# Optimization experiments

Measured on AMD Instinct MI355X. Metric: run time of the kernel, lower is better.

## Reference

```python
import jax, jax.numpy as jnp
import numpy as np

H = 128  # hidden_size = dims[0]
F = 64   # input_size = input_shape[1]
L = 3    # num_layers = len(dims)
B, T = 128, 512


def _gru_layer(x, w_ih, w_hh, b_ih, b_hh):
    """PyTorch-style GRU layer. x: [S, N, in]. Returns (ys [S,N,H], h_T [N,H])."""
    # Precompute input projections for all steps at once: [S, N, 3H]
    px = jnp.einsum('sni,gi->sng', x, w_ih) + b_ih

    def step(h, p):
        gh = h @ w_hh.T + b_hh            # [N, 3H]
        pr, pz, pn = jnp.split(p, 3, axis=-1)
        gr, gz, gn = jnp.split(gh, 3, axis=-1)
        r = jax.nn.sigmoid(pr + gr)
        z = jax.nn.sigmoid(pz + gz)
        n = jnp.tanh(pn + r * gn)
        h_new = (1.0 - z) * n + z * h
        return h_new, h_new

    h0 = jnp.zeros((x.shape[1], w_hh.shape[1]), dtype=x.dtype)
    hT, ys = jax.lax.scan(step, h0, px)
    return ys, hT


def setup_inputs() -> dict:
    key = jax.random.key(0)
    ks = jax.random.split(key, 1 + 4 * L)
    d = {"inp": jax.random.normal(ks[0], (B, T, F), dtype=jnp.float32)}
    k = 1.0 / np.sqrt(H)  # torch default uniform init bound
    for l in range(L):
        in_dim = F if l == 0 else H
        d[f"w_ih_{l}"] = jax.random.uniform(ks[1 + 4 * l + 0], (3 * H, in_dim), jnp.float32, -k, k)
        d[f"w_hh_{l}"] = jax.random.uniform(ks[1 + 4 * l + 1], (3 * H, H), jnp.float32, -k, k)
        d[f"b_ih_{l}"] = jax.random.uniform(ks[1 + 4 * l + 2], (3 * H,), jnp.float32, -k, k)
        d[f"b_hh_{l}"] = jax.random.uniform(ks[1 + 4 * l + 3], (3 * H,), jnp.float32, -k, k)
    return d


def reference(inp, w_ih_0, w_hh_0, b_ih_0, b_hh_0,
              w_ih_1, w_hh_1, b_ih_1, b_hh_1,
              w_ih_2, w_hh_2, b_ih_2, b_hh_2):
    shape = inp.shape
    # torch: reshape to [-1, T, F]; nn.GRU here has batch_first=False (positional-arg bug),
    # so the scan runs over dim 0 (length B) with dim 1 (T) as the GRU batch.
    x = inp.reshape(-1, shape[-2], shape[-1])  # [S=B, N=T, F]
    layers = [(w_ih_0, w_hh_0, b_ih_0, b_hh_0),
              (w_ih_1, w_hh_1, b_ih_1, b_hh_1),
              (w_ih_2, w_hh_2, b_ih_2, b_hh_2)]
    for w_ih, w_hh, b_ih, b_hh in layers:
        x, _ = _gru_layer(x, w_ih, w_hh, b_ih, b_hh)
    # final=False branch: reshape per-step outputs to shape[:-1] + [-1]
    return x.reshape(shape[:-1] + (-1,))
```

## Files before the change

kernel.cpp:

```cpp
#include <hip/hip_runtime.h>

namespace {

constexpr int NTH = 512;
constexpr int NB  = 512;
constexpr int HID = 128;
constexpr int G3  = 384;
constexpr int SS  = 128;
constexpr int CH  = 20;

typedef float f32x2 __attribute__((ext_vector_type(2)));
typedef float f32x4 __attribute__((ext_vector_type(4)));

__device__ __forceinline__ void pk_fma_acc(f32x2& acc, f32x2 a, f32x2 b) {
    asm("v_pk_fma_f32 %0, %1, %2, %0" : "+v"(acc) : "v"(a), "v"(b));
}

template <int CTRL>
__device__ __forceinline__ float add_dpp(float v) {
    int moved = __builtin_amdgcn_update_dpp(0, __float_as_int(v), CTRL, 0xf, 0xf, true);
    return v + __int_as_float(moved);
}

__device__ __forceinline__ float wave_red8(float v) {
    v = add_dpp<0x111>(v);
    v = add_dpp<0x112>(v);
    v = add_dpp<0x114>(v);
    return v;
}

__device__ __forceinline__ float dot4acc(float4 a, float4 b, float acc) {
    acc = fmaf(a.x, b.x, acc);
    acc = fmaf(a.y, b.y, acc);
    acc = fmaf(a.z, b.z, acc);
    acc = fmaf(a.w, b.w, acc);
    return acc;
}

__device__ __forceinline__ float fsigmoid(float x) {
    x = fminf(fmaxf(x, -30.f), 30.f);
    return 1.f / (1.f + __expf(-x));
}

__device__ __forceinline__ float ftanh(float x) {
    x = fminf(fmaxf(x, -15.f), 15.f);
    const float e = __expf(2.f * x);
    return 1.f - 2.f / (e + 1.f);
}

constexpr int BKG = 32;
constexpr int TSTR = 132;

__global__ __launch_bounds__(256, 4) void px_gemm(
    const float* __restrict__ A,
    const float* __restrict__ W,
    const float* __restrict__ bih,
    const float* __restrict__ bhh,
    float* __restrict__ px,
    int kin)
{
    __shared__ __align__(16) float At[BKG * TSTR];
    __shared__ __align__(16) float Wt[BKG * TSTR];

    const int tid = threadIdx.x;
    const int m0  = blockIdx.x * 128;
    const int g0  = blockIdx.y * 128;
    const int tr  = tid >> 4;
    const int tc  = tid & 15;

    f32x2 acc2[8][4];
    #pragma unroll
    for (int i = 0; i < 8; ++i)
        #pragma unroll
        for (int j = 0; j < 4; ++j) acc2[i][j] = f32x2{0.f, 0.f};

    const int srow = tid >> 3;
    const int sf4  = (tid & 7) * 4;

    for (int kt = 0; kt < kin; kt += BKG) {
        #pragma unroll
        for (int p = 0; p < 4; ++p) {
            const int r = p * 32 + srow;
            const float4 va = *reinterpret_cast<const float4*>(A + (size_t)(m0 + r) * kin + kt + sf4);
            At[(sf4 + 0) * TSTR + r] = va.x;
            At[(sf4 + 1) * TSTR + r] = va.y;
            At[(sf4 + 2) * TSTR + r] = va.z;
            At[(sf4 + 3) * TSTR + r] = va.w;
            const float4 vw = *reinterpret_cast<const float4*>(W + (size_t)(g0 + r) * kin + kt + sf4);
            Wt[(sf4 + 0) * TSTR + r] = vw.x;
            Wt[(sf4 + 1) * TSTR + r] = vw.y;
            Wt[(sf4 + 2) * TSTR + r] = vw.z;
            Wt[(sf4 + 3) * TSTR + r] = vw.w;
        }
        __syncthreads();

        #pragma unroll 8
        for (int kk = 0; kk < BKG; ++kk) {
            const float4 a0 = *reinterpret_cast<const float4*>(&At[kk * TSTR + tr * 8]);
            const float4 a1 = *reinterpret_cast<const float4*>(&At[kk * TSTR + tr * 8 + 4]);
            const float4 w0 = *reinterpret_cast<const float4*>(&Wt[kk * TSTR + tc * 8]);
            const float4 w1 = *reinterpret_cast<const float4*>(&Wt[kk * TSTR + tc * 8 + 4]);
            const f32x2 wp[4] = { f32x2{w0.x, w0.y}, f32x2{w0.z, w0.w},
                                  f32x2{w1.x, w1.y}, f32x2{w1.z, w1.w} };
            const float ar[8] = { a0.x, a0.y, a0.z, a0.w, a1.x, a1.y, a1.z, a1.w };
            #pragma unroll
            for (int i = 0; i < 8; ++i) {
                const f32x2 av = f32x2{ar[i], ar[i]};
                #pragma unroll
                for (int j = 0; j < 4; ++j)
                    pk_fma_acc(acc2[i][j], av, wp[j]);
            }
        }
        __syncthreads();
    }

    const int gbase = g0 + tc * 8;
    const bool addz = (g0 < 256);
    float4 b0 = *reinterpret_cast<const float4*>(bih + gbase);
    float4 b1 = *reinterpret_cast<const float4*>(bih + gbase + 4);
    if (addz) {
        const float4 h0 = *reinterpret_cast<const float4*>(bhh + gbase);
        const float4 h1 = *reinterpret_cast<const float4*>(bhh + gbase + 4);
        b0.x += h0.x; b0.y += h0.y; b0.z += h0.z; b0.w += h0.w;
        b1.x += h1.x; b1.y += h1.y; b1.z += h1.z; b1.w += h1.w;
    }
    #pragma unroll
    for (int i = 0; i < 8; ++i) {
        const int m = m0 + tr * 8 + i;
        float4 o0, o1;
        o0.x = acc2[i][0].x + b0.x; o0.y = acc2[i][0].y + b0.y;
        o0.z = acc2[i][1].x + b0.z; o0.w = acc2[i][1].y + b0.w;
        o1.x = acc2[i][2].x + b1.x; o1.y = acc2[i][2].y + b1.y;
        o1.z = acc2[i][3].x + b1.z; o1.w = acc2[i][3].y + b1.w;
        *reinterpret_cast<float4*>(px + (size_t)m * G3 + gbase)     = o0;
        *reinterpret_cast<float4*>(px + (size_t)m * G3 + gbase + 4) = o1;
    }
}

__global__ __launch_bounds__(NTH, 4) void gru_rec(
    const float* __restrict__ px,
    const float* __restrict__ whh,
    const float* __restrict__ bhh,
    float* __restrict__ yd)
{
    __shared__ __align__(16) float hb[8 * CH];
    __shared__ float ghl[G3];
    __shared__ float bhn[HID];

    const int tid  = threadIdx.x;
    const int kgrp = tid & 7;
    const int gt   = tid >> 3;
    const int g0   = gt * 6;
    const int row  = blockIdx.x;

    f32x4 wv[24];
    #pragma unroll
    for (int gg = 0; gg < 6; ++gg)
        #pragma unroll
        for (int q = 0; q < 4; ++q)
            wv[gg * 4 + q] = *reinterpret_cast<const f32x4*>(
                whh + (size_t)(g0 + gg) * HID + kgrp * 16 + q * 4);
    #pragma unroll
    for (int i = 0; i < 24; ++i) asm volatile("" : "+v"(wv[i]));

    for (int i = tid; i < HID; i += NTH) bhn[i] = bhh[256 + i];
    for (int i = tid; i < 8 * CH; i += NTH) hb[i] = 0.f;
    __syncthreads();

    float pxr = 0.f, pxz = 0.f, pxn = 0.f;
    if (tid < HID) {
        const float* p0 = px + (size_t)row * G3 + tid;
        pxr = p0[0]; pxz = p0[128]; pxn = p0[256];
    }

    for (int s = 0; s < SS; ++s) {
        if (tid >= 128 && tid < 256) {
            const int j = tid - 128;
            if (s > 0)
                yd[((size_t)(s - 1) * NB + row) * HID + j] = hb[(j >> 4) * CH + (j & 15)];
        }
        float nxr = 0.f, nxz = 0.f, nxn = 0.f;
        if (tid < HID && s + 1 < SS) {
            const float* p1 = px + ((size_t)(s + 1) * NB + row) * G3 + tid;
            nxr = p1[0]; nxz = p1[128]; nxn = p1[256];
        }

        f32x2 acc[6];
        #pragma unroll
        for (int gg = 0; gg < 6; ++gg) acc[gg] = f32x2{0.f, 0.f};
        #pragma unroll
        for (int q = 0; q < 4; ++q) {
            const f32x4 h4 = *reinterpret_cast<const f32x4*>(&hb[kgrp * CH + q * 4]);
            const f32x2 hlo = h4.xy;
            const f32x2 hhi = h4.zw;
            #pragma unroll
            for (int gg = 0; gg < 6; ++gg) {
                pk_fma_acc(acc[gg], hlo, wv[gg * 4 + q].xy);
                pk_fma_acc(acc[gg], hhi, wv[gg * 4 + q].zw);
            }
        }
        #pragma unroll
        for (int gg = 0; gg < 6; ++gg) {
            const float r = wave_red8(acc[gg].x + acc[gg].y);
            if (kgrp == 7) ghl[g0 + gg] = r;
        }
        __syncthreads();

        if (tid < HID) {
            const float ghr = ghl[tid];
            const float ghz = ghl[tid + 128];
            const float ghn = ghl[tid + 256] + bhn[tid];
            const float r  = fsigmoid(pxr + ghr);
            const float z  = fsigmoid(pxz + ghz);
            const float nn = ftanh(pxn + r * ghn);
            const int hoff = (tid >> 4) * CH + (tid & 15);
            const float hold = hb[hoff];
            hb[hoff] = (1.f - z) * nn + z * hold;
            pxr = nxr; pxz = nxz; pxn = nxn;
        }
        __syncthreads();
    }

    if (tid >= 128 && tid < 256) {
        const int j = tid - 128;
        yd[((size_t)(SS - 1) * NB + row) * HID + j] = hb[(j >> 4) * CH + (j & 15)];
    }
}

__global__ __launch_bounds__(NTH) void gru3_fused(
    const float* __restrict__ xin,
    const float* __restrict__ wih0, const float* __restrict__ whh0,
    const float* __restrict__ bih0, const float* __restrict__ bhh0,
    const float* __restrict__ wih1, const float* __restrict__ whh1,
    const float* __restrict__ bih1, const float* __restrict__ bhh1,
    const float* __restrict__ wih2, const float* __restrict__ whh2,
    const float* __restrict__ bih2, const float* __restrict__ bhh2,
    float* __restrict__ out)
{
    __shared__ __align__(16) float xb[2][2 * 8 * CH];
    __shared__ __align__(16) float hb[2 * 8 * CH];
    __shared__ float pxl[2][G3];
    __shared__ float ghl[2][G3];
    __shared__ float bsum[2 * HID];
    __shared__ float bin_[HID];
    __shared__ float bhn_[HID];

    const int tid  = threadIdx.x;
    const int kgrp = tid & 7;
    const int gt   = tid >> 3;
    const int g0   = gt * 6;
    const int row0 = blockIdx.x * 2;

    float4 wih[6][4];
    float4 whh[6][4];

    for (int layer = 0; layer < 3; ++layer) {
        const float *wi, *wh, *bi, *bh, *xs;
        float* yd;
        int kin;
        if (layer == 0)      { wi = wih0; wh = whh0; bi = bih0; bh = bhh0; xs = xin; yd = out; kin = 64;  }
        else if (layer == 1) { wi = wih1; wh = whh1; bi = bih1; bh = bhh1; xs = out; yd = out; kin = HID; }
        else                 { wi = wih2; wh = whh2; bi = bih2; bh = bhh2; xs = out; yd = out; kin = HID; }

        #pragma unroll
        for (int gg = 0; gg < 6; ++gg) {
            const int g = g0 + gg;
            #pragma unroll
            for (int q = 0; q < 4; ++q) {
                const int k = kgrp * 16 + q * 4;
                whh[gg][q] = *reinterpret_cast<const float4*>(wh + g * HID + k);
                if (k < kin)
                    wih[gg][q] = *reinterpret_cast<const float4*>(wi + g * kin + k);
                else
                    wih[gg][q] = make_float4(0.f, 0.f, 0.f, 0.f);
            }
        }

        for (int i = tid; i < 2 * HID; i += NTH) bsum[i] = bi[i] + bh[i];
        for (int i = tid; i < HID; i += NTH) { bin_[i] = bi[256 + i]; bhn_[i] = bh[256 + i]; }
        for (int i = tid; i < 2 * 8 * CH; i += NTH) { hb[i] = 0.f; xb[0][i] = 0.f; xb[1][i] = 0.f; }
        __syncthreads();
        if (tid < 256) {
            const int n = tid >> 7, j = tid & 127;
            if (j < kin)
                xb[0][n * (8 * CH) + (j >> 4) * CH + (j & 15)] = xs[(0 * NB + row0 + n) * kin + j];
        }
        __syncthreads();

        float ypend = 0.f;
        bool  have_y = false;

        for (int s = 0; s < SS; ++s) {
            float xpref = 0.f;
            if (tid >= 256) {
                const int t2 = tid - 256;
                const int n = t2 >> 7, j = t2 & 127;
                if (s + 1 < SS && j < kin)
                    xpref = xs[((s + 1) * NB + row0 + n) * kin + j];
            } else if (have_y) {
                const int n = tid >> 7, j = tid & 127;
                yd[((s - 1) * NB + row0 + n) * HID + j] = ypend;
            }

            float accp[2][6], accg[2][6];
            #pragma unroll
            for (int n = 0; n < 2; ++n)
                #pragma unroll
                for (int gg = 0; gg < 6; ++gg) { accp[n][gg] = 0.f; accg[n][gg] = 0.f; }

            const float* xcur = xb[s & 1];
            #pragma unroll
            for (int q = 0; q < 4; ++q) {
                const int off = kgrp * CH + q * 4;
                const float4 x0 = *reinterpret_cast<const float4*>(xcur + off);
                const float4 x1 = *reinterpret_cast<const float4*>(xcur + 8 * CH + off);
                const float4 h0 = *reinterpret_cast<const float4*>(hb + off);
                const float4 h1 = *reinterpret_cast<const float4*>(hb + 8 * CH + off);
                #pragma unroll
                for (int gg = 0; gg < 6; ++gg) {
                    accp[0][gg] = dot4acc(x0, wih[gg][q], accp[0][gg]);
                    accp[1][gg] = dot4acc(x1, wih[gg][q], accp[1][gg]);
                    accg[0][gg] = dot4acc(h0, whh[gg][q], accg[0][gg]);
                    accg[1][gg] = dot4acc(h1, whh[gg][q], accg[1][gg]);
                }
            }

            #pragma unroll
            for (int n = 0; n < 2; ++n)
                #pragma unroll
                for (int gg = 0; gg < 6; ++gg) {
                    const float rp = wave_red8(accp[n][gg]);
                    const float rg = wave_red8(accg[n][gg]);
                    if (kgrp == 7) { pxl[n][g0 + gg] = rp; ghl[n][g0 + gg] = rg; }
                }
            __syncthreads();

            if (tid < 256) {
                const int n = tid >> 7, j = tid & 127;
                const float pr = pxl[n][j]       + ghl[n][j]       + bsum[j];
                const float pz = pxl[n][j + 128] + ghl[n][j + 128] + bsum[j + 128];
                const float gn = ghl[n][j + 256] + bhn_[j];
                const float pn = pxl[n][j + 256] + bin_[j];
                const float r  = fsigmoid(pr);
                const float z  = fsigmoid(pz);
                const float nn = ftanh(pn + r * gn);
                const int hoff = n * (8 * CH) + (j >> 4) * CH + (j & 15);
                const float hold = hb[hoff];
                const float hnew = (1.f - z) * nn + z * hold;
                hb[hoff] = hnew;
                ypend = hnew;
                have_y = true;
            } else {
                const int t2 = tid - 256;
                const int n = t2 >> 7, j = t2 & 127;
                if (s + 1 < SS && j < kin)
                    xb[(s + 1) & 1][n * (8 * CH) + (j >> 4) * CH + (j & 15)] = xpref;
            }
            __syncthreads();
        }

        if (tid < 256) {
            const int n = tid >> 7, j = tid & 127;
            yd[((SS - 1) * NB + row0 + n) * HID + j] = ypend;
        }
        __syncthreads();
    }
}

}

extern "C" void kernel_launch(void* const* d_in, const int* in_sizes, int n_in,
                              void* d_out, int out_size, void* d_ws, size_t ws_size,
                              hipStream_t stream)
{
    (void)in_sizes; (void)n_in; (void)out_size;
    const float* xin = (const float*)d_in[0];
    const float* wih[3] = { (const float*)d_in[1], (const float*)d_in[5], (const float*)d_in[9]  };
    const float* whh[3] = { (const float*)d_in[2], (const float*)d_in[6], (const float*)d_in[10] };
    const float* bih[3] = { (const float*)d_in[3], (const float*)d_in[7], (const float*)d_in[11] };
    const float* bhh[3] = { (const float*)d_in[4], (const float*)d_in[8], (const float*)d_in[12] };
    float* out = (float*)d_out;

    const size_t need = (size_t)SS * NB * G3 * sizeof(float);
    if (ws_size >= need) {
        float* px = (float*)d_ws;
        for (int l = 0; l < 3; ++l) {
            const float* A = (l == 0) ? xin : out;
            const int kin = (l == 0) ? 64 : HID;
            px_gemm<<<dim3((SS * NB) / 128, 3), dim3(256), 0, stream>>>(
                A, wih[l], bih[l], bhh[l], px, kin);
            gru_rec<<<dim3(NB), dim3(NTH), 0, stream>>>(px, whh[l], bhh[l], out);
        }
    } else {
        gru3_fused<<<dim3(NB / 2), dim3(NTH), 0, stream>>>(
            xin, wih[0], whh[0], bih[0], bhh[0],
            wih[1], whh[1], bih[1], bhh[1],
            wih[2], whh[2], bih[2], bhh[2], out);
    }
}
```

Baseline: 782.6 us.

## Use split-fp16 MFMA for GRU recurrence with 16 rows per block

Replaces the per-row scalar packed-FMA recurrence kernel with an MFMA kernel in which each block handles 16 batch rows. W_hh and the hidden state are each split into fp16 hi and lo parts, and three MFMA passes (hi*hi, hi*lo, lo*hi) keep near-fp32 accuracy. The hidden state goes through double-buffered, XOR-swizzled LDS, and px is prefetched two steps ahead. The grid shrinks from 512 to 32 blocks, which leaves most of the device's compute units idle. The sigmoid/tanh input clamping is also removed.

```diff
diff --git a/kernel.cpp b/kernel.cpp
--- a/kernel.cpp
+++ b/kernel.cpp
@@ -9,8 +9,10 @@
 constexpr int SS  = 128;
 constexpr int CH  = 20;
 
-typedef float f32x2 __attribute__((ext_vector_type(2)));
-typedef float f32x4 __attribute__((ext_vector_type(4)));
+typedef float    f32x2 __attribute__((ext_vector_type(2)));
+typedef float    f32x4 __attribute__((ext_vector_type(4)));
+typedef _Float16 f16;
+typedef f16      f16x8 __attribute__((ext_vector_type(8)));
 
 __device__ __forceinline__ void pk_fma_acc(f32x2& acc, f32x2 a, f32x2 b) {
     asm("v_pk_fma_f32 %0, %1, %2, %0" : "+v"(acc) : "v"(a), "v"(b));
@@ -21,7 +23,6 @@
     int moved = __builtin_amdgcn_update_dpp(0, __float_as_int(v), CTRL, 0xf, 0xf, true);
     return v + __int_as_float(moved);
 }
-
 __device__ __forceinline__ float wave_red8(float v) {
     v = add_dpp<0x111>(v);
     v = add_dpp<0x112>(v);
@@ -37,27 +38,23 @@
     return acc;
 }
 
-__device__ __forceinline__ float fsigmoid(float x) {
-    x = fminf(fmaxf(x, -30.f), 30.f);
-    return 1.f / (1.f + __expf(-x));
-}
-
-__device__ __forceinline__ float ftanh(float x) {
-    x = fminf(fmaxf(x, -15.f), 15.f);
-    const float e = __expf(2.f * x);
-    return 1.f - 2.f / (e + 1.f);
+__device__ __forceinline__ float fsig(float x)  { return 1.f / (1.f + __expf(-x)); }
+__device__ __forceinline__ float ftanh_(float x){ const float e = __expf(2.f * x); return 1.f - 2.f / (e + 1.f); }
+
+__device__ __forceinline__ f16x8 zero8() {
+    f16x8 z;
+    #pragma unroll
+    for (int e = 0; e < 8; ++e) z[e] = (f16)0.f;
+    return z;
 }
 
 constexpr int BKG = 32;
 constexpr int TSTR = 132;
 
 __global__ __launch_bounds__(256, 4) void px_gemm(
-    const float* __restrict__ A,
-    const float* __restrict__ W,
-    const float* __restrict__ bih,
-    const float* __restrict__ bhh,
-    float* __restrict__ px,
-    int kin)
+    const float* __restrict__ A, const float* __restrict__ W,
+    const float* __restrict__ bih, const float* __restrict__ bhh,
+    float* __restrict__ px, int kin)
 {
     __shared__ __align__(16) float At[BKG * TSTR];
     __shared__ __align__(16) float Wt[BKG * TSTR];
@@ -137,93 +134,123 @@
     }
 }
 
-__global__ __launch_bounds__(NTH, 4) void gru_rec(
+__global__ __launch_bounds__(NTH) void gru_rec_mfma(
     const float* __restrict__ px,
     const float* __restrict__ whh,
     const float* __restrict__ bhh,
     float* __restrict__ yd)
 {
-    __shared__ __align__(16) float hb[8 * CH];
-    __shared__ float ghl[G3];
-    __shared__ float bhn[HID];
+    __shared__ _Float16 hlds[2][2][16 * HID];
 
     const int tid  = threadIdx.x;
-    const int kgrp = tid & 7;
-    const int gt   = tid >> 3;
-    const int g0   = gt * 6;
-    const int row  = blockIdx.x;
-
-    f32x4 wv[24];
-    #pragma unroll
-    for (int gg = 0; gg < 6; ++gg)
-        #pragma unroll
-        for (int q = 0; q < 4; ++q)
-            wv[gg * 4 + q] = *reinterpret_cast<const f32x4*>(
-                whh + (size_t)(g0 + gg) * HID + kgrp * 16 + q * 4);
-    #pragma unroll
-    for (int i = 0; i < 24; ++i) asm volatile("" : "+v"(wv[i]));
-
-    for (int i = tid; i < HID; i += NTH) bhn[i] = bhh[256 + i];
-    for (int i = tid; i < 8 * CH; i += NTH) hb[i] = 0.f;
-    __syncthreads();
-
-    float pxr = 0.f, pxz = 0.f, pxn = 0.f;
-    if (tid < HID) {
-        const float* p0 = px + (size_t)row * G3 + tid;
-        pxr = p0[0]; pxz = p0[128]; pxn = p0[256];
-    }
+    const int lane = tid & 63;
+    const int w    = tid >> 6;
+    const int l15  = lane & 15;
+    const int q    = lane >> 4;
+    const int colc = w * 16 + l15;
+    const int row0 = blockIdx.x * 16;
+
+    f16x8 Whi[3][4], Wlo[3][4];
+    #pragma unroll
+    for (int g = 0; g < 3; ++g) {
+        const int jrow = g * HID + colc;
+        #pragma unroll
+        for (int kt = 0; kt < 4; ++kt) {
+            const float* src = whh + (size_t)jrow * HID + kt * 32 + q * 8;
+            const float4 a = *reinterpret_cast<const float4*>(src);
+            const float4 b = *reinterpret_cast<const float4*>(src + 4);
+            const float v[8] = {a.x, a.y, a.z, a.w, b.x, b.y, b.z, b.w};
+            f16x8 hi, lo;
+            #pragma unroll
+            for (int e = 0; e < 8; ++e) {
+                const f16 h = (f16)v[e];
+                hi[e] = h;
+                lo[e] = (f16)(v[e] - (float)h);
+            }
+            Whi[g][kt] = hi;
+            Wlo[g][kt] = lo;
+        }
+    }
+    const float bhn = bhh[256 + colc];
+
+    float hstate[4] = {0.f, 0.f, 0.f, 0.f};
+    f16x8 Ahi[4], Alo[4];
+    #pragma unroll
+    for (int kt = 0; kt < 4; ++kt) { Ahi[kt] = zero8(); Alo[kt] = zero8(); }
+
+    const float* pxbase = px + (size_t)(row0 + q * 4) * G3 + colc;
+    float* ybase = yd + (size_t)(row0 + q * 4) * HID + colc;
+
+    float pxc[12], pxn[12];
+    #pragma unroll
+    for (int g = 0; g < 3; ++g)
+        #pragma unroll
+        for (int r = 0; r < 4; ++r) {
+            pxc[g * 4 + r] = pxbase[(size_t)r * G3 + g * HID];
+            pxn[g * 4 + r] = pxbase[(size_t)NB * G3 + (size_t)r * G3 + g * HID];
+        }
 
     for (int s = 0; s < SS; ++s) {
-        if (tid >= 128 && tid < 256) {
-            const int j = tid - 128;
-            if (s > 0)
-                yd[((size_t)(s - 1) * NB + row) * HID + j] = hb[(j >> 4) * CH + (j & 15)];
-        }
-        float nxr = 0.f, nxz = 0.f, nxn = 0.f;
-        if (tid < HID && s + 1 < SS) {
-            const float* p1 = px + ((size_t)(s + 1) * NB + row) * G3 + tid;
-            nxr = p1[0]; nxz = p1[128]; nxn = p1[256];
-        }
-
-        f32x2 acc[6];
-        #pragma unroll
-        for (int gg = 0; gg < 6; ++gg) acc[gg] = f32x2{0.f, 0.f};
-        #pragma unroll
-        for (int q = 0; q < 4; ++q) {
-            const f32x4 h4 = *reinterpret_cast<const f32x4*>(&hb[kgrp * CH + q * 4]);
-            const f32x2 hlo = h4.xy;
-            const f32x2 hhi = h4.zw;
-            #pragma unroll
-            for (int gg = 0; gg < 6; ++gg) {
-                pk_fma_acc(acc[gg], hlo, wv[gg * 4 + q].xy);
-                pk_fma_acc(acc[gg], hhi, wv[gg * 4 + q].zw);
-            }
-        }
-        #pragma unroll
-        for (int gg = 0; gg < 6; ++gg) {
-            const float r = wave_red8(acc[gg].x + acc[gg].y);
-            if (kgrp == 7) ghl[g0 + gg] = r;
-        }
-        __syncthreads();
-
-        if (tid < HID) {
-            const float ghr = ghl[tid];
-            const float ghz = ghl[tid + 128];
-            const float ghn = ghl[tid + 256] + bhn[tid];
-            const float r  = fsigmoid(pxr + ghr);
-            const float z  = fsigmoid(pxz + ghz);
-            const float nn = ftanh(pxn + r * ghn);
-            const int hoff = (tid >> 4) * CH + (tid & 15);
-            const float hold = hb[hoff];
-            hb[hoff] = (1.f - z) * nn + z * hold;
-            pxr = nxr; pxz = nxz; pxn = nxn;
-        }
-        __syncthreads();
-    }
-
-    if (tid >= 128 && tid < 256) {
-        const int j = tid - 128;
-        yd[((size_t)(SS - 1) * NB + row) * HID + j] = hb[(j >> 4) * CH + (j & 15)];
+        f32x4 accR = {0.f, 0.f, 0.f, 0.f};
+        f32x4 accZ = {0.f, 0.f, 0.f, 0.f};
+        f32x4 accN = {0.f, 0.f, 0.f, 0.f};
+        #pragma unroll
+        for (int kt = 0; kt < 4; ++kt) {
+            accR = __builtin_amdgcn_mfma_f32_16x16x32_f16(Ahi[kt], Whi[0][kt], accR, 0, 0, 0);
+            accZ = __builtin_amdgcn_mfma_f32_16x16x32_f16(Ahi[kt], Whi[1][kt], accZ, 0, 0, 0);
+            accN = __builtin_amdgcn_mfma_f32_16x16x32_f16(Ahi[kt], Whi[2][kt], accN, 0, 0, 0);
+        }
+        #pragma unroll
+        for (int kt = 0; kt < 4; ++kt) {
+            accR = __builtin_amdgcn_mfma_f32_16x16x32_f16(Ahi[kt], Wlo[0][kt], accR, 0, 0, 0);
+            accZ = __builtin_amdgcn_mfma_f32_16x16x32_f16(Ahi[kt], Wlo[1][kt], accZ, 0, 0, 0);
+            accN = __builtin_amdgcn_mfma_f32_16x16x32_f16(Ahi[kt], Wlo[2][kt], accN, 0, 0, 0);
+        }
+        #pragma unroll
+        for (int kt = 0; kt < 4; ++kt) {
+            accR = __builtin_amdgcn_mfma_f32_16x16x32_f16(Alo[kt], Whi[0][kt], accR, 0, 0, 0);
+            accZ = __builtin_amdgcn_mfma_f32_16x16x32_f16(Alo[kt], Whi[1][kt], accZ, 0, 0, 0);
+            accN = __builtin_amdgcn_mfma_f32_16x16x32_f16(Alo[kt], Whi[2][kt], accN, 0, 0, 0);
+        }
+
+        _Float16* wb0 = &hlds[(s + 1) & 1][0][0];
+        _Float16* wb1 = &hlds[(s + 1) & 1][1][0];
+        #pragma unroll
+        for (int r = 0; r < 4; ++r) {
+            const float rr = fsig(pxc[r]     + accR[r]);
+            const float zz = fsig(pxc[4 + r] + accZ[r]);
+            const float nn = ftanh_(pxc[8 + r] + rr * (accN[r] + bhn));
+            const float hn = (1.f - zz) * nn + zz * hstate[r];
+            hstate[r] = hn;
+            ybase[(size_t)s * NB * HID + (size_t)r * HID] = hn;
+            const int m   = q * 4 + r;
+            const int idx = (m * HID + colc) ^ ((m & 7) << 3);
+            const f16 hh = (f16)hn;
+            wb0[idx] = hh;
+            wb1[idx] = (f16)(hn - (float)hh);
+        }
+
+        #pragma unroll
+        for (int i = 0; i < 12; ++i) pxc[i] = pxn[i];
+        if (s + 2 < SS) {
+            const float* pb = pxbase + (size_t)(s + 2) * NB * G3;
+            #pragma unroll
+            for (int g = 0; g < 3; ++g)
+                #pragma unroll
+                for (int r = 0; r < 4; ++r)
+                    pxn[g * 4 + r] = pb[(size_t)r * G3 + g * HID];
+        }
+
+        __syncthreads();
+
+        const _Float16* rb0 = &hlds[(s + 1) & 1][0][0];
+        const _Float16* rb1 = &hlds[(s + 1) & 1][1][0];
+        #pragma unroll
+        for (int kt = 0; kt < 4; ++kt) {
+            const int idx = (l15 * HID + kt * 32 + q * 8) ^ ((l15 & 7) << 3);
+            Ahi[kt] = *reinterpret_cast<const f16x8*>(rb0 + idx);
+            Alo[kt] = *reinterpret_cast<const f16x8*>(rb1 + idx);
+        }
     }
 }
 
@@ -341,9 +368,9 @@
                 const float pz = pxl[n][j + 128] + ghl[n][j + 128] + bsum[j + 128];
                 const float gn = ghl[n][j + 256] + bhn_[j];
                 const float pn = pxl[n][j + 256] + bin_[j];
-                const float r  = fsigmoid(pr);
-                const float z  = fsigmoid(pz);
-                const float nn = ftanh(pn + r * gn);
+                const float r  = fsig(pr);
+                const float z  = fsig(pz);
+                const float nn = ftanh_(pn + r * gn);
                 const int hoff = n * (8 * CH) + (j >> 4) * CH + (j & 15);
                 const float hold = hb[hoff];
                 const float hnew = (1.f - z) * nn + z * hold;
@@ -389,7 +416,7 @@
             const int kin = (l == 0) ? 64 : HID;
             px_gemm<<<dim3((SS * NB) / 128, 3), dim3(256), 0, stream>>>(
                 A, wih[l], bih[l], bhh[l], px, kin);
-            gru_rec<<<dim3(NB), dim3(NTH), 0, stream>>>(px, whh[l], bhh[l], out);
+            gru_rec_mfma<<<dim3(NB / 16), dim3(NTH), 0, stream>>>(px, whh[l], bhh[l], out);
         }
     } else {
         gru3_fused<<<dim3(NB / 2), dim3(NTH), 0, stream>>>(
```

Result: slower. 915.9 us (+17.0%).
